# Performance work log

Hardware: AMD Instinct MI355X
Metric: run time of the kernel (lower is better)

Reference implementation:

```python
import jax, jax.numpy as jnp
import numpy as np

NODE_DIM = 16
N_VERTS = 54
SEAT_DIM = 4
HIDDEN = 128
N = 16384
EPS = 1e-5


def _layer_norm(x, g, b):
    m = jnp.mean(x, axis=-1, keepdims=True)
    v = jnp.var(x, axis=-1, keepdims=True)
    return (x - m) * jax.lax.rsqrt(v + EPS) * g + b


def setup_inputs() -> dict:
    key = jax.random.key(0)
    ks = jax.random.split(key, 32)
    h = HIDDEN
    mlp_in = h * 3 + 8
    d = {
        "X": jax.random.normal(ks[0], (N, N_VERTS, NODE_DIM), dtype=jnp.float32),
        "A_hat": jax.random.uniform(ks[1], (N_VERTS, N_VERTS), dtype=jnp.float32) / N_VERTS,
        "v1_idx": jax.random.randint(ks[2], (N,), 0, N_VERTS),
        "v2_idx": jax.random.randint(ks[3], (N,), 0, N_VERTS),
        "seat": jax.random.randint(ks[4], (N,), 0, SEAT_DIM),
        # conv layer 0: in NODE_DIM -> h
        "conv0_W": jax.random.normal(ks[5], (NODE_DIM, h), dtype=jnp.float32) * 0.1,
        "conv0_b": jnp.zeros((h,), jnp.float32),
        "ln0_g": jnp.ones((h,), jnp.float32),
        "ln0_b": jnp.zeros((h,), jnp.float32),
        # conv layers 1,2: h -> h
        "conv1_W": jax.random.normal(ks[6], (h, h), dtype=jnp.float32) * 0.05,
        "conv1_b": jnp.zeros((h,), jnp.float32),
        "ln1_g": jnp.ones((h,), jnp.float32),
        "ln1_b": jnp.zeros((h,), jnp.float32),
        "conv2_W": jax.random.normal(ks[7], (h, h), dtype=jnp.float32) * 0.05,
        "conv2_b": jnp.zeros((h,), jnp.float32),
        "ln2_g": jnp.ones((h,), jnp.float32),
        "ln2_b": jnp.zeros((h,), jnp.float32),
        "seat_emb": jax.random.normal(ks[8], (SEAT_DIM + 1, 8), dtype=jnp.float32),
        "mlp_W1": jax.random.normal(ks[9], (mlp_in, 128), dtype=jnp.float32) * 0.05,
        "mlp_b1": jnp.zeros((128,), jnp.float32),
        "mlp_W2": jax.random.normal(ks[10], (128, 64), dtype=jnp.float32) * 0.1,
        "mlp_b2": jnp.zeros((64,), jnp.float32),
        "mlp_W3": jax.random.normal(ks[11], (64, 1), dtype=jnp.float32) * 0.1,
        "mlp_b3": jnp.zeros((1,), jnp.float32),
        # rank head: mlp_in -> 64 -> 1 (sigmoid)
        "rank_W1": jax.random.normal(ks[12], (mlp_in, 64), dtype=jnp.float32) * 0.05,
        "rank_b1": jnp.zeros((64,), jnp.float32),
        "rank_W2": jax.random.normal(ks[13], (64, 1), dtype=jnp.float32) * 0.1,
        "rank_b2": jnp.zeros((1,), jnp.float32),
    }
    return d


def reference(X, A_hat, v1_idx, v2_idx, seat,
              conv0_W, conv0_b, ln0_g, ln0_b,
              conv1_W, conv1_b, ln1_g, ln1_b,
              conv2_W, conv2_b, ln2_g, ln2_b,
              seat_emb,
              mlp_W1, mlp_b1, mlp_W2, mlp_b2, mlp_W3, mlp_b3,
              rank_W1, rank_b1, rank_W2, rank_b2):
    convs = [(conv0_W, conv0_b, ln0_g, ln0_b),
             (conv1_W, conv1_b, ln1_g, ln1_b),
             (conv2_W, conv2_b, ln2_g, ln2_b)]
    H = X  # (N, 54, in_dim)
    for i, (W, b, g, beta) in enumerate(convs):
        HW = jnp.einsum('nvd,dk->nvk', H, W) + b          # linear
        out = jnp.einsum('ij,njk->nik', A_hat, HW)         # adjacency mix
        H_new = jax.nn.relu(_layer_norm(out, g, beta))     # dropout = identity (eval)
        H = H + H_new if i > 0 else H_new
    n = H.shape[0]
    rows = jnp.arange(n)
    v1_emb = H[rows, v1_idx]                               # (N, h)
    v2_emb = H[rows, v2_idx]
    gpool = jnp.mean(H, axis=1)                            # (N, h)
    s_emb = seat_emb[jnp.clip(seat, 0, SEAT_DIM - 1)]      # (N, 8)
    h = jnp.concatenate([v1_emb, v2_emb, gpool, s_emb], axis=-1)
    z = jax.nn.relu(h @ mlp_W1 + mlp_b1)
    z = jax.nn.relu(z @ mlp_W2 + mlp_b2)
    win_logit = z @ mlp_W3 + mlp_b3                        # (N, 1)
    r = jax.nn.relu(h @ rank_W1 + rank_b1)
    rank_pred = jax.nn.sigmoid(r @ rank_W2 + rank_b2)      # (N, 1)
    return (win_logit, rank_pred)
```

## Files before the change

### kernel.cpp

```cpp
#include <hip/hip_runtime.h>
#include <hip/hip_bf16.h>
#include <math.h>


typedef __bf16 bf16x8 __attribute__((ext_vector_type(8)));
typedef float  f32x4  __attribute__((ext_vector_type(4)));
typedef unsigned int u32x4 __attribute__((ext_vector_type(4)));
typedef unsigned int u32x2 __attribute__((ext_vector_type(2)));

#define DEVINL __device__ __forceinline__
#define HROW 400

DEVINL unsigned bfr(float x) {
    unsigned u = __float_as_uint(x);
    return (u + 0x7fffu + ((u >> 16) & 1u)) >> 16;
}
DEVINL unsigned pk2(float a, float b) {
    float2 f; f.x = a; f.y = b;
    __hip_bfloat162 h = __float22bfloat162_rn(f);
    unsigned u;
    __builtin_memcpy(&u, &h, sizeof(u));
    return u;
}
DEVINL unsigned short bf1(float x) {
    return (unsigned short)bfr(x);
}

DEVINL f32x4 MFMA(u32x4 a, u32x4 b, f32x4 c) {
    return __builtin_amdgcn_mfma_f32_16x16x32_bf16(
        __builtin_bit_cast(bf16x8, a), __builtin_bit_cast(bf16x8, b), c, 0, 0, 0);
}

#define TS 36
#define HS 68
DEVINL int TROW(int r) { return r * TS + ((r >> 3) & 1) * 4; }

DEVINL void conv12g(f32x4 (&rg)[8], const unsigned* Hlds,
                    const u32x4* __restrict__ Wp, int w, int g, int c15, int l)
{
    #pragma unroll
    for (int i = 0; i < 8; ++i) rg[i] = (f32x4){0.f, 0.f, 0.f, 0.f};
    #pragma unroll
    for (int ks = 0; ks < 4; ++ks) {
        u32x4 wf0 = Wp[((2 * w + 0) * 4 + ks) * 64 + l];
        u32x4 wf1 = Wp[((2 * w + 1) * 4 + ks) * 64 + l];
        u32x4 hb[4];
        #pragma unroll
        for (int ut = 0; ut < 4; ++ut)
            hb[ut] = *(const u32x4*)&Hlds[(ut * 16 + c15) * HS + ks * 16 + g * 4];
        #pragma unroll
        for (int ut = 0; ut < 4; ++ut) {
            rg[ut]     = MFMA(wf0, hb[ut], rg[ut]);
            rg[4 + ut] = MFMA(wf1, hb[ut], rg[4 + ut]);
        }
    }
}

DEVINL void conv_epi(const f32x4 (&rg)[8], unsigned short* TldsH, const float* bias,
                     int w, int g, int c15)
{
    #pragma unroll
    for (int m2 = 0; m2 < 2; ++m2) {
        const int chb = (2 * w + m2) * 16;
        f32x4 bb = *(const f32x4*)&bias[chb + g * 4];
        #pragma unroll
        for (int ut = 0; ut < 4; ++ut) {
            const int u = ut * 16 + c15;
            #pragma unroll
            for (int r = 0; r < 4; ++r)
                TldsH[TROW(chb + g * 4 + r) * 2 + u] = bf1(rg[m2 * 4 + ut][r] + bb[r]);
        }
    }
}

DEVINL void do_mix(f32x4 (&rg)[8], const unsigned* Tlds, const unsigned* Amlds,
                   int w, int g, int c15)
{
    const int vrow = (w * 16 + c15) * TS + g * 4;
    u32x4 bf0 = *(const u32x4*)&Amlds[vrow];
    u32x4 bf1v = *(const u32x4*)&Amlds[vrow + 16];
    #pragma unroll
    for (int mt = 0; mt < 8; ++mt) {
        const int crow = TROW(mt * 16 + c15) + g * 4;
        u32x4 a0 = *(const u32x4*)&Tlds[crow];
        u32x4 a1 = *(const u32x4*)&Tlds[crow + 16];
        f32x4 a = {0.f, 0.f, 0.f, 0.f};
        a = MFMA(a0, bf0, a);
        a = MFMA(a1, bf1v, a);
        rg[mt] = a;
    }
}

DEVINL void mix_epi(const f32x4 (&rg)[8], float (&Rf)[8][4], unsigned* Hlds,
                    const float* gam, const float* bet, bool resid, bool writeH,
                    int w, int g, int c15)
{
    float s = 0.f, q = 0.f;
    #pragma unroll
    for (int mt = 0; mt < 8; ++mt)
        #pragma unroll
        for (int r = 0; r < 4; ++r) { float x = rg[mt][r]; s += x; q = fmaf(x, x, q); }
    s += __shfl_xor(s, 16); s += __shfl_xor(s, 32);
    q += __shfl_xor(q, 16); q += __shfl_xor(q, 32);
    const float m   = s * (1.f / 128.f);
    const float var = q * (1.f / 128.f) - m * m;
    const float rs  = rsqrtf(var + 1e-5f);
    const int v = w * 16 + c15;
    #pragma unroll
    for (int mt = 0; mt < 8; ++mt) {
        f32x4 gc = *(const f32x4*)&gam[mt * 16 + g * 4];
        f32x4 bc = *(const f32x4*)&bet[mt * 16 + g * 4];
        #pragma unroll
        for (int r = 0; r < 4; ++r) {
            float val = fmaxf((rg[mt][r] - m) * rs * gc[r] + bc[r], 0.f);
            if (resid) val += Rf[mt][r];
            Rf[mt][r] = val;
        }
        if (writeH) {
            u32x2 pr;
            pr[0] = pk2(Rf[mt][0], Rf[mt][1]);
            pr[1] = pk2(Rf[mt][2], Rf[mt][3]);
            *(u32x2*)&Hlds[v * HS + mt * 8 + g * 2] = pr;
        }
    }
}

__global__ __launch_bounds__(256, 3) void gcn_mfma(
    const float* __restrict__ X, const float* __restrict__ A,
    const int* __restrict__ v1i, const int* __restrict__ v2i, const int* __restrict__ seat,
    const float* __restrict__ W0, const float* __restrict__ b0v,
    const float* __restrict__ g0v, const float* __restrict__ be0,
    const unsigned* __restrict__ W1G, const float* __restrict__ b1v,
    const float* __restrict__ g1v, const float* __restrict__ be1,
    const unsigned* __restrict__ W2G, const float* __restrict__ b2v,
    const float* __restrict__ g2v, const float* __restrict__ be2,
    const float* __restrict__ semb, float* __restrict__ hws, int spb)
{
    __shared__ unsigned Tlds[128 * TS + 4];
    __shared__ unsigned Hlds[64 * HS];
    __shared__ unsigned Amlds[64 * TS];
    __shared__ float    PrmL[9][128];
    __shared__ float    Sm[4][128];
    __shared__ unsigned long long WpS[2];

    const int tid = threadIdx.x;
    const int l = tid & 63, w = tid >> 6, g = l >> 4, c15 = l & 15;

    if (tid < 128) {
        const int c = tid;
        PrmL[0][c] = b0v[c]; PrmL[1][c] = b1v[c]; PrmL[2][c] = b2v[c];
        PrmL[3][c] = g0v[c]; PrmL[4][c] = g1v[c]; PrmL[5][c] = g2v[c];
        PrmL[6][c] = be0[c]; PrmL[7][c] = be1[c]; PrmL[8][c] = be2[c];
    }
    if (tid == 0) {
        WpS[0] = (unsigned long long)W1G;
        WpS[1] = (unsigned long long)W2G;
    }
    for (int p = tid; p < 64 * TS; p += 256) {
        const int v = p / TS, uc = p % TS;
        unsigned val = 0u;
        if (v < 54 && uc < 27) {
            const int u = uc * 2;
            const float a0 = A[v * 54 + u];
            const float a1 = (u + 1 < 54) ? A[v * 54 + u + 1] : 0.f;
            val = pk2(a0, a1);
        }
        Amlds[p] = val;
    }

    u32x4 W0f[2];
    #pragma unroll
    for (int m2 = 0; m2 < 2; ++m2) {
        const int ch = (2 * w + m2) * 16 + c15;
        unsigned t0[4];
        #pragma unroll
        for (int jj = 0; jj < 4; ++jj) {
            const int k = g * 8 + 2 * jj;
            t0[jj] = (g < 2) ? pk2(W0[k * 128 + ch], W0[(k + 1) * 128 + ch]) : 0u;
        }
        W0f[m2] = (u32x4){t0[0], t0[1], t0[2], t0[3]};
    }
    __syncthreads();

    float Rf[8][4];
    f32x4 rg[8];

    #pragma unroll 1
    for (int it = 0; it < spb; ++it) {
        const int n = blockIdx.x + gridDim.x * it;

        const u32x4* W1p = (const u32x4*)(((volatile unsigned long long*)WpS)[0]);
        const u32x4* W2p = (const u32x4*)(((volatile unsigned long long*)WpS)[1]);

        #pragma unroll
        for (int i = 0; i < 8; ++i) rg[i] = (f32x4){0.f, 0.f, 0.f, 0.f};
        #pragma unroll
        for (int ut = 0; ut < 4; ++ut) {
            const int u = ut * 16 + c15;
            u32x4 xb = (u32x4){0u, 0u, 0u, 0u};
            if (g < 2 && u < 54) {
                const f32x4* xp = (const f32x4*)(X + (size_t)n * 864 + u * 16 + g * 8);
                f32x4 f0 = xp[0], f1 = xp[1];
                xb = (u32x4){pk2(f0[0], f0[1]), pk2(f0[2], f0[3]),
                             pk2(f1[0], f1[1]), pk2(f1[2], f1[3])};
            }
            #pragma unroll
            for (int m2 = 0; m2 < 2; ++m2)
                rg[m2 * 4 + ut] = MFMA(W0f[m2], xb, rg[m2 * 4 + ut]);
        }
        conv_epi(rg, (unsigned short*)Tlds, &PrmL[0][0], w, g, c15);
        __syncthreads();
        do_mix(rg, Tlds, Amlds, w, g, c15);
        mix_epi(rg, Rf, Hlds, &PrmL[3][0], &PrmL[6][0], false, true, w, g, c15);
        __syncthreads();

        conv12g(rg, Hlds, W1p, w, g, c15, l);
        conv_epi(rg, (unsigned short*)Tlds, &PrmL[1][0], w, g, c15);
        __syncthreads();
        do_mix(rg, Tlds, Amlds, w, g, c15);
        mix_epi(rg, Rf, Hlds, &PrmL[4][0], &PrmL[7][0], true, true, w, g, c15);
        __syncthreads();

        conv12g(rg, Hlds, W2p, w, g, c15, l);
        conv_epi(rg, (unsigned short*)Tlds, &PrmL[2][0], w, g, c15);
        __syncthreads();
        do_mix(rg, Tlds, Amlds, w, g, c15);
        mix_epi(rg, Rf, Hlds, &PrmL[5][0], &PrmL[8][0], true, true, w, g, c15);
        __syncthreads();

        const int v1 = v1i[n], v2 = v2i[n];
        int st = seat[n];
        st = st < 0 ? 0 : (st > 3 ? 3 : st);
        float* hr = hws + (size_t)n * HROW;
        const int v = w * 16 + c15;

        if (v == v1 || v == v2) {
            #pragma unroll
            for (int mt = 0; mt < 8; ++mt) {
                f32x4 t;
                #pragma unroll
                for (int r = 0; r < 4; ++r) t[r] = Rf[mt][r];
                if (v == v1) *(f32x4*)&hr[mt * 16 + g * 4] = t;
                if (v == v2) *(f32x4*)&hr[128 + mt * 16 + g * 4] = t;
            }
        }

        {
            const int pair = tid & 63;
            const int nv = (w == 3) ? 6 : 16;
            float s0 = 0.f, s1 = 0.f;
            const unsigned* hb = &Hlds[(w * 16) * HS + pair];
            for (int r = 0; r < nv; ++r) {
                const unsigned u = hb[r * HS];
                s0 += __uint_as_float(u << 16);
                s1 += __uint_as_float(u & 0xffff0000u);
            }
            Sm[w][2 * pair]     = s0;
            Sm[w][2 * pair + 1] = s1;
        }
        __syncthreads();
        if (tid < 128) {
            const float mn = (Sm[0][tid] + Sm[1][tid] + Sm[2][tid] + Sm[3][tid]) * (1.f / 54.f);
            hr[256 + tid] = mn;
        }
        if (tid < 8)       hr[384 + tid] = semb[st * 8 + tid];
        else if (tid < 16) hr[384 + tid] = 0.f;
    }
}

__global__ void head_frag_init(const float* __restrict__ mW1,
                               const float* __restrict__ rW1,
                               const float* __restrict__ mW2,
                               const float* __restrict__ W1t,
                               const float* __restrict__ W2t,
                               unsigned* __restrict__ W1h, unsigned* __restrict__ W1l,
                               unsigned* __restrict__ R1h, unsigned* __restrict__ W2h,
                               unsigned* __restrict__ W1G, unsigned* __restrict__ W2G)
{
    const int t = blockIdx.x * 256 + threadIdx.x;
    if (t < 13 * 128 * 16) {
        const int j = t & 3, g = (t >> 2) & 3, col = (t >> 4) & 127, ks = t >> 11;
        const int k = ks * 32 + g * 8 + 2 * j;
        const float w0 = (k < 392)     ? mW1[k * 128 + col]       : 0.f;
        const float w1 = (k + 1 < 392) ? mW1[(k + 1) * 128 + col] : 0.f;
        const unsigned h0 = bfr(w0), h1 = bfr(w1);
        const float l0 = w0 - __uint_as_float(h0 << 16);
        const float l1 = w1 - __uint_as_float(h1 << 16);
        const int idx = ((ks * 8 + (col >> 4)) * 64 + g * 16 + (col & 15)) * 4 + j;
        W1h[idx] = h0 | (h1 << 16);
        W1l[idx] = pk2(l0, l1);
    }
    if (t < 13 * 64 * 16) {
        const int j = t & 3, g = (t >> 2) & 3, col = (t >> 4) & 63, ks = t >> 10;
        const int k = ks * 32 + g * 8 + 2 * j;
        const float w0 = (k < 392)     ? rW1[k * 64 + col]       : 0.f;
        const float w1 = (k + 1 < 392) ? rW1[(k + 1) * 64 + col] : 0.f;
        const int idx = ((ks * 4 + (col >> 4)) * 64 + g * 16 + (col & 15)) * 4 + j;
        R1h[idx] = pk2(w0, w1);
    }
    if (t < 4 * 64 * 16) {
        const int j = t & 3, g = (t >> 2) & 3, col = (t >> 4) & 63, ks2 = t >> 10;
        const int k = ks2 * 32 + g * 8 + 2 * j;
        const int idx = ((ks2 * 4 + (col >> 4)) * 64 + g * 16 + (col & 15)) * 4 + j;
        W2h[idx] = pk2(mW2[k * 64 + col], mW2[(k + 1) * 64 + col]);
    }
    if (t < 8 * 4 * 64 * 4) {
        const int j = t & 3, lane = (t >> 2) & 63, ks = (t >> 8) & 3, ct = t >> 10;
        const int g2 = lane >> 4, c15 = lane & 15;
        const int k = ks * 32 + g2 * 8 + 2 * j;
        const int ch = ct * 16 + c15;
        W1G[t] = pk2(W1t[k * 128 + ch], W1t[(k + 1) * 128 + ch]);
        W2G[t] = pk2(W2t[k * 128 + ch], W2t[(k + 1) * 128 + ch]);
    }
}

__global__ __launch_bounds__(256, 2) void head_mfma(
    const float* __restrict__ hws,
    const unsigned* __restrict__ W1hG, const unsigned* __restrict__ W1lG,
    const unsigned* __restrict__ R1hG, const unsigned* __restrict__ W2hG,
    const float* __restrict__ mb1, const float* __restrict__ mb2,
    const float* __restrict__ mW3, const float* __restrict__ mb3,
    const float* __restrict__ rb1, const float* __restrict__ rW2,
    const float* __restrict__ rb2,
    float* __restrict__ out, int N)
{
    __shared__ u32x4 Zh[16 * 64];

    const int tid = threadIdx.x, l = tid & 63, w = tid >> 6, g = l >> 4, c15 = l & 15;
    const int row = blockIdx.x * 64 + w * 16 + c15;

    const u32x4* W1h4 = (const u32x4*)W1hG;
    const u32x4* W1l4 = (const u32x4*)W1lG;
    const u32x4* R1h4 = (const u32x4*)R1hG;
    const u32x4* W2h4 = (const u32x4*)W2hG;

    f32x4 z1[8], rr[4];
    #pragma unroll
    for (int i = 0; i < 8; ++i) z1[i] = (f32x4){0.f, 0.f, 0.f, 0.f};
    #pragma unroll
    for (int i = 0; i < 4; ++i) rr[i] = (f32x4){0.f, 0.f, 0.f, 0.f};

    #pragma unroll 1
    for (int ks = 0; ks < 13; ++ks) {
        const float* hp = hws + (size_t)row * HROW + ks * 32 + g * 8;
        f32x4 f0 = *(const f32x4*)hp, f1 = *(const f32x4*)(hp + 4);
        float vv[8] = {f0[0], f0[1], f0[2], f0[3], f1[0], f1[1], f1[2], f1[3]};
        unsigned th[4], tl[4];
        #pragma unroll
        for (int jj = 0; jj < 4; ++jj) {
            unsigned ha = bfr(vv[2 * jj]), hb = bfr(vv[2 * jj + 1]);
            th[jj] = ha | (hb << 16);
            tl[jj] = pk2(vv[2 * jj] - __uint_as_float(ha << 16),
                         vv[2 * jj + 1] - __uint_as_float(hb << 16));
        }
        u32x4 ah = (u32x4){th[0], th[1], th[2], th[3]};
        u32x4 al = (u32x4){tl[0], tl[1], tl[2], tl[3]};
        #pragma unroll
        for (int nt = 0; nt < 8; ++nt) {
            u32x4 bh = W1h4[(ks * 8 + nt) * 64 + l];
            u32x4 bl = W1l4[(ks * 8 + nt) * 64 + l];
            f32x4 a = z1[nt];
            a = MFMA(ah, bh, a); a = MFMA(ah, bl, a); a = MFMA(al, bh, a);
            z1[nt] = a;
        }
        #pragma unroll
        for (int nt = 0; nt < 4; ++nt)
            rr[nt] = MFMA(ah, R1h4[(ks * 4 + nt) * 64 + l], rr[nt]);
    }

    float rp[4] = {0.f, 0.f, 0.f, 0.f};
    #pragma unroll
    for (int nt = 0; nt < 4; ++nt) {
        int c = nt * 16 + c15;
        float rb = rb1[c], rw = rW2[c];
        #pragma unroll
        for (int r = 0; r < 4; ++r) rp[r] += fmaxf(rr[nt][r] + rb, 0.f) * rw;
    }
    #pragma unroll
    for (int r = 0; r < 4; ++r) {
        float p = rp[r];
        #pragma unroll
        for (int m = 1; m <= 8; m <<= 1) p += __shfl_xor(p, m);
        if (c15 == 0) {
            int orow = blockIdx.x * 64 + w * 16 + g * 4 + r;
            out[N + orow] = 1.f / (1.f + expf(-(p + rb2[0])));
        }
    }

    {
        unsigned short* zp = (unsigned short*)Zh;
        #pragma unroll
        for (int nt = 0; nt < 8; ++nt) {
            int c = nt * 16 + c15;
            float bb = mb1[c];
            #pragma unroll
            for (int r = 0; r < 4; ++r) {
                float v = fmaxf(z1[nt][r] + bb, 0.f);
                int lanep = ((nt * 2 + (c15 >> 3)) & 3) * 16 + g * 4 + r;
                zp[((w * 4 + (nt >> 1)) * 64 + lanep) * 8 + (c15 & 7)] = (unsigned short)bfr(v);
            }
        }
    }
    __syncthreads();

    f32x4 z2a[4];
    #pragma unroll
    for (int i = 0; i < 4; ++i) z2a[i] = (f32x4){0.f, 0.f, 0.f, 0.f};
    #pragma unroll
    for (int ks2 = 0; ks2 < 4; ++ks2) {
        u32x4 za = Zh[(w * 4 + ks2) * 64 + l];
        #pragma unroll
        for (int nt2 = 0; nt2 < 4; ++nt2)
            z2a[nt2] = MFMA(za, W2h4[(ks2 * 4 + nt2) * 64 + l], z2a[nt2]);
    }
    float wp[4] = {0.f, 0.f, 0.f, 0.f};
    #pragma unroll
    for (int nt2 = 0; nt2 < 4; ++nt2) {
        int c = nt2 * 16 + c15;
        float bb = mb2[c], w3 = mW3[c];
        #pragma unroll
        for (int r = 0; r < 4; ++r) wp[r] += fmaxf(z2a[nt2][r] + bb, 0.f) * w3;
    }
    #pragma unroll
    for (int r = 0; r < 4; ++r) {
        float p = wp[r];
        #pragma unroll
        for (int m = 1; m <= 8; m <<= 1) p += __shfl_xor(p, m);
        if (c15 == 0) {
            int orow = blockIdx.x * 64 + w * 16 + g * 4 + r;
            out[orow] = p + mb3[0];
        }
    }
}

extern "C" void kernel_launch(void* const* d_in, const int* in_sizes, int n_in,
                              void* d_out, int out_size, void* d_ws, size_t ws_size,
                              hipStream_t stream) {
    const float* X        = (const float*)d_in[0];
    const float* A        = (const float*)d_in[1];
    const int*   v1_idx   = (const int*)d_in[2];
    const int*   v2_idx   = (const int*)d_in[3];
    const int*   seat     = (const int*)d_in[4];
    const float* W0       = (const float*)d_in[5];
    const float* b0       = (const float*)d_in[6];
    const float* g0       = (const float*)d_in[7];
    const float* be0      = (const float*)d_in[8];
    const float* W1       = (const float*)d_in[9];
    const float* b1       = (const float*)d_in[10];
    const float* g1       = (const float*)d_in[11];
    const float* be1      = (const float*)d_in[12];
    const float* W2       = (const float*)d_in[13];
    const float* b2       = (const float*)d_in[14];
    const float* g2       = (const float*)d_in[15];
    const float* be2      = (const float*)d_in[16];
    const float* seat_emb = (const float*)d_in[17];
    const float* mW1      = (const float*)d_in[18];
    const float* mb1      = (const float*)d_in[19];
    const float* mW2      = (const float*)d_in[20];
    const float* mb2      = (const float*)d_in[21];
    const float* mW3      = (const float*)d_in[22];
    const float* mb3      = (const float*)d_in[23];
    const float* rW1      = (const float*)d_in[24];
    const float* rb1      = (const float*)d_in[25];
    const float* rW2      = (const float*)d_in[26];
    const float* rb2      = (const float*)d_in[27];

    const int N = in_sizes[2];
    float* out = (float*)d_out;

    float*    hws = (float*)d_ws;
    unsigned* W1h = (unsigned*)((char*)d_ws + (size_t)N * HROW * 4);
    unsigned* W1l = W1h + 26624;
    unsigned* R1h = W1l + 26624;
    unsigned* W2h = R1h + 13312;
    unsigned* W1G = W2h + 4096;
    unsigned* W2G = W1G + 8192;

    head_frag_init<<<104, 256, 0, stream>>>(mW1, rW1, mW2, W1, W2,
                                            W1h, W1l, R1h, W2h, W1G, W2G);

    const int spb = 8;
    const int gridA = N / spb;
    gcn_mfma<<<gridA, 256, 0, stream>>>(
        X, A, v1_idx, v2_idx, seat,
        W0, b0, g0, be0, W1G, b1, g1, be1, W2G, b2, g2, be2,
        seat_emb, hws, spb);

    const int gridB = N / 64;
    head_mfma<<<gridB, 256, 0, stream>>>(
        hws, W1h, W1l, R1h, W2h,
        mb1, mb2, mW3, mb3, rb1, rW2, rb2, out, N);
}
```

Measured before the change: 328.3 us.

## Move adjacency fragments and conv biases into registers to cut LDS and raise occupancy

```diff
diff --git a/kernel.cpp b/kernel.cpp
--- a/kernel.cpp
+++ b/kernel.cpp
@@ -56,37 +56,33 @@
     }
 }
 
-DEVINL void conv_epi(const f32x4 (&rg)[8], unsigned short* TldsH, const float* bias,
-                     int w, int g, int c15)
+DEVINL void conv_epi(const f32x4 (&rg)[8], unsigned short* TldsH,
+                     const f32x4 (&bb)[2], int w, int g, int c15)
 {
     #pragma unroll
     for (int m2 = 0; m2 < 2; ++m2) {
         const int chb = (2 * w + m2) * 16;
-        f32x4 bb = *(const f32x4*)&bias[chb + g * 4];
         #pragma unroll
         for (int ut = 0; ut < 4; ++ut) {
             const int u = ut * 16 + c15;
             #pragma unroll
             for (int r = 0; r < 4; ++r)
-                TldsH[TROW(chb + g * 4 + r) * 2 + u] = bf1(rg[m2 * 4 + ut][r] + bb[r]);
-        }
-    }
-}
-
-DEVINL void do_mix(f32x4 (&rg)[8], const unsigned* Tlds, const unsigned* Amlds,
-                   int w, int g, int c15)
-{
-    const int vrow = (w * 16 + c15) * TS + g * 4;
-    u32x4 bf0 = *(const u32x4*)&Amlds[vrow];
-    u32x4 bf1v = *(const u32x4*)&Amlds[vrow + 16];
+                TldsH[TROW(chb + g * 4 + r) * 2 + u] = bf1(rg[m2 * 4 + ut][r] + bb[m2][r]);
+        }
+    }
+}
+
+DEVINL void do_mix(f32x4 (&rg)[8], const unsigned* Tlds,
+                   u32x4 bfA0, u32x4 bfA1, int g, int c15)
+{
     #pragma unroll
     for (int mt = 0; mt < 8; ++mt) {
         const int crow = TROW(mt * 16 + c15) + g * 4;
         u32x4 a0 = *(const u32x4*)&Tlds[crow];
         u32x4 a1 = *(const u32x4*)&Tlds[crow + 16];
         f32x4 a = {0.f, 0.f, 0.f, 0.f};
-        a = MFMA(a0, bf0, a);
-        a = MFMA(a1, bf1v, a);
+        a = MFMA(a0, bfA0, a);
+        a = MFMA(a1, bfA1, a);
         rg[mt] = a;
     }
 }
@@ -125,8 +121,8 @@
     }
 }
 
-__global__ __launch_bounds__(256, 3) void gcn_mfma(
-    const float* __restrict__ X, const float* __restrict__ A,
+__global__ __launch_bounds__(256, 4) void gcn_mfma(
+    const float* __restrict__ X, const unsigned* __restrict__ AmG,
     const int* __restrict__ v1i, const int* __restrict__ v2i, const int* __restrict__ seat,
     const float* __restrict__ W0, const float* __restrict__ b0v,
     const float* __restrict__ g0v, const float* __restrict__ be0,
@@ -138,35 +134,23 @@
 {
     __shared__ unsigned Tlds[128 * TS + 4];
     __shared__ unsigned Hlds[64 * HS];
-    __shared__ unsigned Amlds[64 * TS];
-    __shared__ float    PrmL[9][128];
-    __shared__ float    Sm[4][128];
+    __shared__ float    Gb[6][128];
     __shared__ unsigned long long WpS[2];
+
+    float* SmF = (float*)Tlds;
 
     const int tid = threadIdx.x;
     const int l = tid & 63, w = tid >> 6, g = l >> 4, c15 = l & 15;
 
     if (tid < 128) {
         const int c = tid;
-        PrmL[0][c] = b0v[c]; PrmL[1][c] = b1v[c]; PrmL[2][c] = b2v[c];
-        PrmL[3][c] = g0v[c]; PrmL[4][c] = g1v[c]; PrmL[5][c] = g2v[c];
-        PrmL[6][c] = be0[c]; PrmL[7][c] = be1[c]; PrmL[8][c] = be2[c];
+        Gb[0][c] = g0v[c]; Gb[1][c] = g1v[c]; Gb[2][c] = g2v[c];
+        Gb[3][c] = be0[c]; Gb[4][c] = be1[c]; Gb[5][c] = be2[c];
     }
     if (tid == 0) {
         WpS[0] = (unsigned long long)W1G;
         WpS[1] = (unsigned long long)W2G;
     }
-    for (int p = tid; p < 64 * TS; p += 256) {
-        const int v = p / TS, uc = p % TS;
-        unsigned val = 0u;
-        if (v < 54 && uc < 27) {
-            const int u = uc * 2;
-            const float a0 = A[v * 54 + u];
-            const float a1 = (u + 1 < 54) ? A[v * 54 + u + 1] : 0.f;
-            val = pk2(a0, a1);
-        }
-        Amlds[p] = val;
-    }
 
     u32x4 W0f[2];
     #pragma unroll
@@ -180,6 +164,17 @@
         }
         W0f[m2] = (u32x4){t0[0], t0[1], t0[2], t0[3]};
     }
+    f32x4 Bv[3][2];
+    #pragma unroll
+    for (int m2 = 0; m2 < 2; ++m2) {
+        const int ch4 = (2 * w + m2) * 16 + g * 4;
+        Bv[0][m2] = *(const f32x4*)&b0v[ch4];
+        Bv[1][m2] = *(const f32x4*)&b1v[ch4];
+        Bv[2][m2] = *(const f32x4*)&b2v[ch4];
+    }
+    const u32x4* AmG4 = (const u32x4*)AmG;
+    u32x4 AmF0 = AmG4[(w * 2 + 0) * 64 + l];
+    u32x4 AmF1 = AmG4[(w * 2 + 1) * 64 + l];
     __syncthreads();
 
     float Rf[8][4];
@@ -208,24 +203,24 @@
             for (int m2 = 0; m2 < 2; ++m2)
                 rg[m2 * 4 + ut] = MFMA(W0f[m2], xb, rg[m2 * 4 + ut]);
         }
-        conv_epi(rg, (unsigned short*)Tlds, &PrmL[0][0], w, g, c15);
-        __syncthreads();
-        do_mix(rg, Tlds, Amlds, w, g, c15);
-        mix_epi(rg, Rf, Hlds, &PrmL[3][0], &PrmL[6][0], false, true, w, g, c15);
+        conv_epi(rg, (unsigned short*)Tlds, Bv[0], w, g, c15);
+        __syncthreads();
+        do_mix(rg, Tlds, AmF0, AmF1, g, c15);
+        mix_epi(rg, Rf, Hlds, &Gb[0][0], &Gb[3][0], false, true, w, g, c15);
         __syncthreads();
 
         conv12g(rg, Hlds, W1p, w, g, c15, l);
-        conv_epi(rg, (unsigned short*)Tlds, &PrmL[1][0], w, g, c15);
-        __syncthreads();
-        do_mix(rg, Tlds, Amlds, w, g, c15);
-        mix_epi(rg, Rf, Hlds, &PrmL[4][0], &PrmL[7][0], true, true, w, g, c15);
+        conv_epi(rg, (unsigned short*)Tlds, Bv[1], w, g, c15);
+        __syncthreads();
+        do_mix(rg, Tlds, AmF0, AmF1, g, c15);
+        mix_epi(rg, Rf, Hlds, &Gb[1][0], &Gb[4][0], true, true, w, g, c15);
         __syncthreads();
 
         conv12g(rg, Hlds, W2p, w, g, c15, l);
-        conv_epi(rg, (unsigned short*)Tlds, &PrmL[2][0], w, g, c15);
-        __syncthreads();
-        do_mix(rg, Tlds, Amlds, w, g, c15);
-        mix_epi(rg, Rf, Hlds, &PrmL[5][0], &PrmL[8][0], true, true, w, g, c15);
+        conv_epi(rg, (unsigned short*)Tlds, Bv[2], w, g, c15);
+        __syncthreads();
+        do_mix(rg, Tlds, AmF0, AmF1, g, c15);
+        mix_epi(rg, Rf, Hlds, &Gb[2][0], &Gb[5][0], true, true, w, g, c15);
         __syncthreads();
 
         const int v1 = v1i[n], v2 = v2i[n];
@@ -255,16 +250,18 @@
                 s0 += __uint_as_float(u << 16);
                 s1 += __uint_as_float(u & 0xffff0000u);
             }
-            Sm[w][2 * pair]     = s0;
-            Sm[w][2 * pair + 1] = s1;
+            SmF[w * 128 + 2 * pair]     = s0;
+            SmF[w * 128 + 2 * pair + 1] = s1;
         }
         __syncthreads();
         if (tid < 128) {
-            const float mn = (Sm[0][tid] + Sm[1][tid] + Sm[2][tid] + Sm[3][tid]) * (1.f / 54.f);
+            const float mn = (SmF[tid] + SmF[128 + tid] + SmF[256 + tid] + SmF[384 + tid])
+                             * (1.f / 54.f);
             hr[256 + tid] = mn;
         }
         if (tid < 8)       hr[384 + tid] = semb[st * 8 + tid];
         else if (tid < 16) hr[384 + tid] = 0.f;
+        __syncthreads();
     }
 }
 
@@ -273,9 +270,11 @@
                                const float* __restrict__ mW2,
                                const float* __restrict__ W1t,
                                const float* __restrict__ W2t,
+                               const float* __restrict__ Amat,
                                unsigned* __restrict__ W1h, unsigned* __restrict__ W1l,
                                unsigned* __restrict__ R1h, unsigned* __restrict__ W2h,
-                               unsigned* __restrict__ W1G, unsigned* __restrict__ W2G)
+                               unsigned* __restrict__ W1G, unsigned* __restrict__ W2G,
+                               unsigned* __restrict__ AmG)
 {
     const int t = blockIdx.x * 256 + threadIdx.x;
     if (t < 13 * 128 * 16) {
@@ -311,6 +310,15 @@
         const int ch = ct * 16 + c15;
         W1G[t] = pk2(W1t[k * 128 + ch], W1t[(k + 1) * 128 + ch]);
         W2G[t] = pk2(W2t[k * 128 + ch], W2t[(k + 1) * 128 + ch]);
+    }
+    if (t < 2048) {
+        const int j = t & 3, lane = (t >> 2) & 63, h = (t >> 8) & 1, wt = t >> 9;
+        const int g2 = lane >> 4, cc = lane & 15;
+        const int v = wt * 16 + cc;
+        const int u = h * 32 + g2 * 8 + 2 * j;
+        const float a0 = (v < 54 && u < 54)     ? Amat[v * 54 + u]     : 0.f;
+        const float a1 = (v < 54 && u + 1 < 54) ? Amat[v * 54 + u + 1] : 0.f;
+        AmG[t] = pk2(a0, a1);
     }
 }
 
@@ -475,14 +483,15 @@
     unsigned* W2h = R1h + 13312;
     unsigned* W1G = W2h + 4096;
     unsigned* W2G = W1G + 8192;
-
-    head_frag_init<<<104, 256, 0, stream>>>(mW1, rW1, mW2, W1, W2,
-                                            W1h, W1l, R1h, W2h, W1G, W2G);
+    unsigned* AmG = W2G + 8192;
+
+    head_frag_init<<<104, 256, 0, stream>>>(mW1, rW1, mW2, W1, W2, A,
+                                            W1h, W1l, R1h, W2h, W1G, W2G, AmG);
 
     const int spb = 8;
     const int gridA = N / spb;
     gcn_mfma<<<gridA, 256, 0, stream>>>(
-        X, A, v1_idx, v2_idx, seat,
+        X, AmG, v1_idx, v2_idx, seat,
         W0, b0, g0, be0, W1G, b1, g1, be1, W2G, b2, g2, be2,
         seat_emb, hws, spb);
 
```

After: 389.1 us. 18.5% more time.
